# Optimization experiments

Measured on AMD Instinct MI355X. Metric: run time of the kernel, lower is better.

## Reference

```python
import jax, jax.numpy as jnp
import numpy as np

NUM_ITER = 5
NUM_SLOTS = 16
INPUT_SIZE = 256
EPS = 1e-8
TAU = 1.0
B, N = 8, 16384


def setup_inputs() -> dict:
    key = jax.random.key(0)
    k1, k2 = jax.random.split(key)
    inputs = jax.random.normal(k1, (B, N, INPUT_SIZE), dtype=jnp.float32)
    # xavier_uniform for a (1, K, D) tensor (torch fan_in=K*D, fan_out=D)
    limit = float(np.sqrt(6.0 / (NUM_SLOTS * INPUT_SIZE + INPUT_SIZE)))
    slot_logits = jax.random.uniform(k2, (1, NUM_SLOTS, INPUT_SIZE),
                                     minval=-limit, maxval=limit, dtype=jnp.float32)
    mixing_coefficients = jnp.full((1, NUM_SLOTS), 1.0 / NUM_SLOTS, dtype=jnp.float32)
    return {"inputs": inputs, "slot_logits": slot_logits,
            "mixing_coefficients": mixing_coefficients}


def reference(inputs, slot_logits, mixing_coefficients):
    Bn, Nn, D = inputs.shape
    theta = jnp.broadcast_to(slot_logits, (Bn, NUM_SLOTS, D))       # (B,K,D)
    pi = jnp.broadcast_to(mixing_coefficients, (Bn, NUM_SLOTS))     # (B,K)
    p = jax.nn.softmax(inputs, axis=-1)                             # (B,N,D), loop-invariant
    for _ in range(NUM_ITER):
        log_q = jax.nn.log_softmax(theta, axis=-1)                  # (B,K,D)
        logits = jnp.einsum('bnd,bkd->bnk', p, log_q)               # (B,N,K)
        logits = logits + jnp.log(pi + EPS)[:, None, :]
        gamma = jax.nn.softmax(logits, axis=-1)                     # (B,N,K)
        pi = gamma.mean(axis=1)                                     # (B,K)
        gamma_sum = gamma.sum(axis=1) + EPS                         # (B,K)
        numerator = jnp.einsum('bnk,bnd->bkd', gamma, inputs)       # (B,K,D)
        theta = numerator / gamma_sum[:, :, None]
    g = jax.random.gumbel(jax.random.key(1), theta.shape, dtype=theta.dtype)
    slots = jax.nn.softmax((theta + g) / TAU, axis=-1)              # (B,K,D)
    return slots
```

## Files before the change

### kernel.cpp

```cpp
#include <hip/hip_runtime.h>
#include <cstdint>
#include <cstddef>

#define BN 8
#define NN 16384
#define DD 256
#define KK 16
#define NITER 5
#define EPSV 1e-8f
#define LOG256 5.545177444479562f
#define PSTR 260
#define TPB 8
#define GG 64

typedef float f32x4 __attribute__((ext_vector_type(4)));
typedef long  i64v;

__device__ __forceinline__ float frcp(float x){ return __builtin_amdgcn_rcpf(x); }
__device__ __forceinline__ float wmax(float v){
  #pragma unroll
  for (int m = 32; m >= 1; m >>= 1) v = fmaxf(v, __shfl_xor(v, m, 64));
  return v;
}
__device__ __forceinline__ float wsum(float v){
  #pragma unroll
  for (int m = 32; m >= 1; m >>= 1) v += __shfl_xor(v, m, 64);
  return v;
}
__device__ __forceinline__ uint32_t pk4_fp8(float a, float b, float c, float d){
  int w = __builtin_amdgcn_cvt_pk_fp8_f32(a, b, 0, false);
  w = __builtin_amdgcn_cvt_pk_fp8_f32(c, d, w, true);
  return (uint32_t)w;
}
__device__ __forceinline__ uint32_t f2bf(float f){
  uint32_t u = __float_as_uint(f);
  return (u + 0x7fffu + ((u >> 16) & 1u)) >> 16;
}
__device__ __forceinline__ uint32_t pk2bf(float a, float b){
  return f2bf(a) | (f2bf(b) << 16);
}
__device__ __forceinline__ float bf2f(uint32_t h){ return __uint_as_float(h << 16); }

__global__ __launch_bounds__(256, 2) void k_prep6(const float* __restrict__ x,
                                                  uint2* __restrict__ pbf8,
                                                  uint2* __restrict__ xbf8,
                                                  float* __restrict__ invs){
  __shared__ float xs[2][32 * PSTR];
  const int b = blockIdx.y;
  const int Sbase = blockIdx.x * TPB;
  const int tid = threadIdx.x;
  const int wave = tid >> 6, lane = tid & 63;
  const float* xb = x + (size_t)b * NN * DD;

  auto stage = [&](int S, int buf){
    #pragma unroll
    for (int r = 0; r < 8; ++r){
      int row = wave * 8 + r;
      const float* gp = xb + ((size_t)S * 32 + row) * DD + lane * 4;
      float* lp = &xs[buf][row * PSTR];
      __builtin_amdgcn_global_load_lds(
          (const __attribute__((address_space(1))) unsigned int*)gp,
          (__attribute__((address_space(3))) unsigned int*)lp, 16, 0, 0);
    }
  };

  stage(Sbase, 0);
  for (int it = 0; it < TPB; ++it){
    const int S = Sbase + it;
    const int cur = it & 1;
    asm volatile("s_waitcnt vmcnt(0)" ::: "memory");
    __builtin_amdgcn_sched_barrier(0);
    __syncthreads();
    if (it + 1 < TPB) stage(S + 1, cur ^ 1);

    {
      int row = 8 * wave + (lane & 7);
      const float* pr = &xs[cur][row * PSTR + (lane >> 3) * 32];
      float a = 0.f;
      #pragma unroll
      for (int i = 0; i < 8; ++i){
        float4 v = *(const float4*)&pr[4 * i];
        a += __expf(v.x) + __expf(v.y) + __expf(v.z) + __expf(v.w);
      }
      a += __shfl_xor(a, 8, 64);
      a += __shfl_xor(a, 16, 64);
      a += __shfl_xor(a, 32, 64);
      if (lane < 8) invs[(size_t)b * NN + S * 32 + 8 * wave + lane] = frcp(a);
    }

    #pragma unroll
    for (int i = 0; i < 4; ++i){
      int p = wave * 4 + i; int c = p >> 3, s = p & 7;
      int rho = lane & 15;
      int n = 8 * (rho >> 2) + 4 * c + (rho & 3);
      int d = 32 * s + 8 * (lane >> 4);
      float4 v0 = *(const float4*)&xs[cur][n * PSTR + d];
      float4 v1 = *(const float4*)&xs[cur][n * PSTR + d + 4];
      uint2 o;
      o.x = pk4_fp8(__expf(v0.x), __expf(v0.y), __expf(v0.z), __expf(v0.w));
      o.y = pk4_fp8(__expf(v1.x), __expf(v1.y), __expf(v1.z), __expf(v1.w));
      pbf8[(((size_t)b * 1024 + (size_t)S * 2 + c) * 8 + s) * 64 + lane] = o;
    }
    #pragma unroll
    for (int i = 0; i < 4; ++i){
      int dt = wave * 4 + i;
      int col = dt * 16 + (lane & 15);
      int g2 = lane >> 4;
      float v[8];
      #pragma unroll
      for (int j = 0; j < 8; ++j) v[j] = xs[cur][(8 * g2 + j) * PSTR + col];
      uint2 o;
      o.x = pk4_fp8(v[0], v[1], v[2], v[3]);
      o.y = pk4_fp8(v[4], v[5], v[6], v[7]);
      xbf8[(((size_t)b * 512 + S) * 16 + dt) * 64 + lane] = o;
    }
    __syncthreads();
  }
}

__global__ __launch_bounds__(256) void k_init6(const float* __restrict__ slot_logits,
                                               const float* __restrict__ mix,
                                               uint8_t* __restrict__ lqf8,
                                               float* __restrict__ logpi){
  int w    = blockIdx.x * 4 + (threadIdx.x >> 6);
  int lane = threadIdx.x & 63;
  int b = w >> 4, k = w & 15;
  const float4* sl = (const float4*)(slot_logits + (size_t)k * DD);
  float4 t = sl[lane];
  float m = wmax(fmaxf(fmaxf(t.x, t.y), fmaxf(t.z, t.w)));
  float s = wsum(__expf(t.x-m) + __expf(t.y-m) + __expf(t.z-m) + __expf(t.w-m));
  float L = m + __logf(s) - LOG256;
  int d0 = lane * 4;
  int ss = d0 >> 5;
  int l2 = (((d0 & 31) >> 3) << 4) + k;
  int jb = d0 & 7;
  uint32_t wv = pk4_fp8(t.x - L, t.y - L, t.z - L, t.w - L);
  *(uint32_t*)(lqf8 + ((((size_t)b * 8 + ss) * 64 + l2) * 8 + jb)) = wv;
  if (lane == 0) logpi[w] = __logf(mix[k] + EPSV);
}

__global__ __launch_bounds__(256, 2) void k_em6(const uint2* __restrict__ pbf8,
                                                const uint2* __restrict__ xbf8,
                                                const uint2* __restrict__ lqf8,
                                                const float* __restrict__ logpi,
                                                const float* __restrict__ invs,
                                                uint16_t* __restrict__ pnumb,
                                                float* __restrict__ ppi){
  __shared__ float sred[KK * DD];
  __shared__ float spi2[16];
  const int b = blockIdx.y, g = blockIdx.x;
  const int tid = threadIdx.x;
  const int wave = tid >> 6, lane = tid & 63;

  i64v lq8[8];
  {
    const uint2* p = lqf8 + (size_t)b * 8 * 64 + lane;
    #pragma unroll
    for (int s = 0; s < 8; ++s){ uint2 t = p[s * 64]; lq8[s] = *(i64v*)&t; }
  }
  const float lpik = logpi[b * KK + (lane & 15)];

  f32x4 acc[16];
  #pragma unroll
  for (int dt = 0; dt < 16; ++dt) acc[dt] = (f32x4){0.f, 0.f, 0.f, 0.f};
  float piacc = 0.f;

  const int S0 = (g * 4 + wave) * 2;
  #pragma unroll
  for (int ssi = 0; ssi < 2; ++ssi){
    const int S = S0 + ssi;
    const uint2* pb = pbf8 + (((size_t)b * 1024 + (size_t)S * 2) * 8) * 64 + lane;
    const uint2* xr = xbf8 + (((size_t)b * 512 + S) * 16) * 64 + lane;

    uint2 pa[16];
    #pragma unroll
    for (int i = 0; i < 16; ++i) pa[i] = pb[(size_t)i * 64];

    float ivs[8];
    {
      const float* ib = invs + (size_t)b * NN + S * 32 + 8 * (lane >> 4);
      #pragma unroll
      for (int j = 0; j < 8; ++j) ivs[j] = ib[j];
    }

    float ga[8];
    #pragma unroll
    for (int c = 0; c < 2; ++c){
      f32x4 lc = (f32x4){0.f, 0.f, 0.f, 0.f};
      #pragma unroll
      for (int s = 0; s < 8; ++s){
        i64v a = *(i64v*)&pa[c * 8 + s];
        lc = __builtin_amdgcn_mfma_f32_16x16x32_fp8_fp8(a, lq8[s], lc, 0, 0, 0);
      }
      #pragma unroll
      for (int r2 = 0; r2 < 4; ++r2){
        float lg = fmaf(lc[r2], ivs[c * 4 + r2], lpik);
        float mx = lg;
        #pragma unroll
        for (int m = 1; m <= 8; m <<= 1) mx = fmaxf(mx, __shfl_xor(mx, m, 64));
        float e = __expf(lg - mx);
        float s2 = e;
        #pragma unroll
        for (int m = 1; m <= 8; m <<= 1) s2 += __shfl_xor(s2, m, 64);
        ga[c * 4 + r2] = e * frcp(s2);
      }
    }
    uint2 gp;
    gp.x = pk4_fp8(ga[0], ga[1], ga[2], ga[3]);
    gp.y = pk4_fp8(ga[4], ga[5], ga[6], ga[7]);
    piacc += __builtin_amdgcn_cvt_f32_fp8((int)gp.x, 0)
           + __builtin_amdgcn_cvt_f32_fp8((int)gp.x, 1)
           + __builtin_amdgcn_cvt_f32_fp8((int)gp.x, 2)
           + __builtin_amdgcn_cvt_f32_fp8((int)gp.x, 3)
           + __builtin_amdgcn_cvt_f32_fp8((int)gp.y, 0)
           + __builtin_amdgcn_cvt_f32_fp8((int)gp.y, 1)
           + __builtin_amdgcn_cvt_f32_fp8((int)gp.y, 2)
           + __builtin_amdgcn_cvt_f32_fp8((int)gp.y, 3);
    i64v gA = *(i64v*)&gp;
    #pragma unroll
    for (int dt = 0; dt < 16; ++dt){
      uint2 xv = xr[(size_t)dt * 64];
      acc[dt] = __builtin_amdgcn_mfma_f32_16x16x32_fp8_fp8(gA, *(i64v*)&xv,
                                                           acc[dt], 0, 0, 0);
    }
  }

  float pk = piacc;
  pk += __shfl_xor(pk, 16, 64);
  pk += __shfl_xor(pk, 32, 64);
  __syncthreads();
  if (wave == 0){
    #pragma unroll
    for (int dt = 0; dt < 16; ++dt)
      #pragma unroll
      for (int r2 = 0; r2 < 4; ++r2)
        sred[(4 * (lane >> 4) + r2) * DD + dt * 16 + (lane & 15)] = acc[dt][r2];
    if (lane < 16) spi2[lane] = pk;
  }
  __syncthreads();
  for (int w = 1; w < 4; ++w){
    if (wave == w){
      #pragma unroll
      for (int dt = 0; dt < 16; ++dt)
        #pragma unroll
        for (int r2 = 0; r2 < 4; ++r2)
          sred[(4 * (lane >> 4) + r2) * DD + dt * 16 + (lane & 15)] += acc[dt][r2];
      if (lane < 16) spi2[lane] += pk;
    }
    __syncthreads();
  }
  uint32_t* dst = (uint32_t*)(pnumb + (size_t)(b * GG + g) * KK * DD);
  #pragma unroll
  for (int j = 0; j < 8; ++j){
    float a = sred[tid * 2 + j * 512];
    float c = sred[tid * 2 + 1 + j * 512];
    dst[tid + j * 256] = pk2bf(a, c);
  }
  if (tid < 16) ppi[(size_t)(b * GG + g) * KK + tid] = spi2[tid];
}

__global__ __launch_bounds__(64) void k_reduce6(const uint16_t* __restrict__ pnumb,
                                                const float* __restrict__ ppi,
                                                float* __restrict__ theta,
                                                uint8_t* __restrict__ lqf8,
                                                float* __restrict__ logpi){
  int w = blockIdx.x;
  int lane = threadIdx.x;
  int b = w >> 4, k = w & 15;
  float4 sum = make_float4(0.f, 0.f, 0.f, 0.f);
  #pragma unroll 4
  for (int g = 0; g < GG; ++g){
    const uint2* p = (const uint2*)(pnumb +
        ((size_t)(b * GG + g) * KK + k) * DD + lane * 4);
    uint2 v = *p;
    sum.x += bf2f(v.x & 0xffffu); sum.y += bf2f(v.x >> 16);
    sum.z += bf2f(v.y & 0xffffu); sum.w += bf2f(v.y >> 16);
  }
  float ps = 0.f;
  for (int g = lane; g < GG; g += 64) ps += ppi[((size_t)b * GG + g) * KK + k];
  ps = wsum(ps);
  float inv = frcp(ps + EPSV);
  float4 th = make_float4(sum.x * inv, sum.y * inv, sum.z * inv, sum.w * inv);
  ((float4*)(theta + (size_t)w * DD))[lane] = th;
  float m = wmax(fmaxf(fmaxf(th.x, th.y), fmaxf(th.z, th.w)));
  float s = wsum(__expf(th.x-m) + __expf(th.y-m) + __expf(th.z-m) + __expf(th.w-m));
  float L = m + __logf(s) - LOG256;
  int d0 = lane * 4;
  int ss = d0 >> 5;
  int l2 = (((d0 & 31) >> 3) << 4) + k;
  int jb = d0 & 7;
  uint32_t wv = pk4_fp8(th.x - L, th.y - L, th.z - L, th.w - L);
  *(uint32_t*)(lqf8 + ((((size_t)b * 8 + ss) * 64 + l2) * 8 + jb)) = wv;
  if (lane == 0) logpi[w] = __logf(ps * (1.0f / NN) + EPSV);
}

__device__ __forceinline__ uint32_t rotl32(uint32_t x, int r){ return (x << r) | (x >> (32 - r)); }
__device__ __forceinline__ void tf2x32(uint32_t k0, uint32_t k1, uint32_t c0, uint32_t c1,
                                       uint32_t& o0, uint32_t& o1){
  uint32_t ks0 = k0, ks1 = k1, ks2 = 0x1BD11BDAu ^ k0 ^ k1;
  uint32_t x0 = c0 + ks0, x1 = c1 + ks1;
  #define RND(r) { x0 += x1; x1 = rotl32(x1, r); x1 ^= x0; }
  RND(13) RND(15) RND(26) RND(6)   x0 += ks1; x1 += ks2 + 1u;
  RND(17) RND(29) RND(16) RND(24)  x0 += ks2; x1 += ks0 + 2u;
  RND(13) RND(15) RND(26) RND(6)   x0 += ks0; x1 += ks1 + 3u;
  RND(17) RND(29) RND(16) RND(24)  x0 += ks1; x1 += ks2 + 4u;
  RND(13) RND(15) RND(26) RND(6)   x0 += ks2; x1 += ks0 + 5u;
  #undef RND
  o0 = x0; o1 = x1;
}

__global__ __launch_bounds__(256) void k_final(const float* __restrict__ theta,
                                               float* __restrict__ out){
  int w    = blockIdx.x * 4 + (threadIdx.x >> 6);
  int lane = threadIdx.x & 63;
  float4 th = ((const float4*)(theta + (size_t)w * DD))[lane];
  int i0 = w * DD + lane * 4;
  float gv[4];
  #pragma unroll
  for (int j = 0; j < 4; ++j){
    uint32_t i = (uint32_t)(i0 + j);
    uint32_t o0, o1;
    tf2x32(0u, 1u, 0u, i, o0, o1);
    uint32_t bits = o0 ^ o1;
    float f = __uint_as_float((bits >> 9) | 0x3f800000u) - 1.0f;
    const float TINY = 1.17549435e-38f;
    float u = fmaxf(f + TINY, TINY);
    gv[j] = -logf(-logf(u));
  }
  float4 y = make_float4(th.x + gv[0], th.y + gv[1], th.z + gv[2], th.w + gv[3]);
  float m = wmax(fmaxf(fmaxf(y.x, y.y), fmaxf(y.z, y.w)));
  float4 e = make_float4(__expf(y.x-m), __expf(y.y-m), __expf(y.z-m), __expf(y.w-m));
  float s = wsum(e.x + e.y + e.z + e.w);
  float inv = 1.0f / s;
  ((float4*)(out + (size_t)w * DD))[lane] =
      make_float4(e.x*inv, e.y*inv, e.z*inv, e.w*inv);
}

__global__ __launch_bounds__(256) void k_fill(float* __restrict__ out, float v){
  out[blockIdx.x * 256 + threadIdx.x] = v;
}

extern "C" void kernel_launch(void* const* d_in, const int* in_sizes, int n_in,
                              void* d_out, int out_size, void* d_ws, size_t ws_size,
                              hipStream_t stream){
  const float* x    = (const float*)d_in[0];
  const float* sl   = (const float*)d_in[1];
  const float* mix  = (const float*)d_in[2];
  float* out = (float*)d_out;
  char* ws = (char*)d_ws;

  const size_t SZ_PBF  = 33554432ull;
  const size_t SZ_XBF  = 33554432ull;
  const size_t SZ_LQF  = 32768ull;
  const size_t SZ_INV  = (size_t)BN*NN*4;
  const size_t SZ_TH   = (size_t)BN*KK*DD*4;
  const size_t SZ_LP   = 512ull;
  const size_t SZ_PNUM = (size_t)BN*GG*KK*DD*2;
  const size_t SZ_PPI  = (size_t)BN*GG*KK*4;
  size_t need = SZ_PBF + SZ_XBF + SZ_LQF + SZ_INV + SZ_TH + SZ_LP + SZ_PNUM + SZ_PPI;

  if (ws_size < need){
    k_fill<<<(BN*KK*DD)/256, 256, 0, stream>>>(out, -9.0f);
    return;
  }
  size_t o = 0;
  uint2*    pbf8  = (uint2*)(ws + o);     o += SZ_PBF;
  uint2*    xbf8  = (uint2*)(ws + o);     o += SZ_XBF;
  uint8_t*  lqf8  = (uint8_t*)(ws + o);   o += SZ_LQF;
  float*    invs  = (float*)(ws + o);     o += SZ_INV;
  float*    theta = (float*)(ws + o);     o += SZ_TH;
  float*    logpi = (float*)(ws + o);     o += SZ_LP;
  uint16_t* pnumb = (uint16_t*)(ws + o);  o += SZ_PNUM;
  float*    ppi   = (float*)(ws + o);

  k_prep6<<<dim3(512 / TPB, BN), 256, 0, stream>>>(x, pbf8, xbf8, invs);
  k_init6<<<(BN*KK)/4, 256, 0, stream>>>(sl, mix, lqf8, logpi);
  for (int it = 0; it < NITER; ++it){
    k_em6    <<<dim3(GG, BN), 256, 0, stream>>>(pbf8, xbf8, (const uint2*)lqf8,
                                                logpi, invs, pnumb, ppi);
    k_reduce6<<<BN*KK, 64, 0, stream>>>(pnumb, ppi, theta, lqf8, logpi);
  }
  k_final<<<(BN*KK)/4, 256, 0, stream>>>(theta, out);
}
```

Baseline: 161.5 us.

## Fuse per-iteration reduction and final softmax into EM kernel via last-block counter

The separate reduce and final kernels are folded into the EM kernel. The last block to finish for each batch, detected with an atomic counter and thread fences, does the cross-block reduction, updates log_q and log_pi, and on the last iteration applies the Gumbel softmax directly. This removes six kernel launches and the theta buffer, at the cost of a serial tail where one block per batch does all 16 row reductions. Separately, the prep kernel drops its LDS double buffering and raises its occupancy hint from 2 to 4 blocks, relying on more resident blocks rather than in-block prefetch to hide load latency.

```diff
diff --git a/kernel.cpp b/kernel.cpp
--- a/kernel.cpp
+++ b/kernel.cpp
@@ -41,41 +41,35 @@
 }
 __device__ __forceinline__ float bf2f(uint32_t h){ return __uint_as_float(h << 16); }
 
-__global__ __launch_bounds__(256, 2) void k_prep6(const float* __restrict__ x,
+__global__ __launch_bounds__(256, 4) void k_prep6(const float* __restrict__ x,
                                                   uint2* __restrict__ pbf8,
                                                   uint2* __restrict__ xbf8,
                                                   float* __restrict__ invs){
-  __shared__ float xs[2][32 * PSTR];
+  __shared__ float xs[32 * PSTR];
   const int b = blockIdx.y;
   const int Sbase = blockIdx.x * TPB;
   const int tid = threadIdx.x;
   const int wave = tid >> 6, lane = tid & 63;
   const float* xb = x + (size_t)b * NN * DD;
 
-  auto stage = [&](int S, int buf){
+  for (int it = 0; it < TPB; ++it){
+    const int S = Sbase + it;
     #pragma unroll
     for (int r = 0; r < 8; ++r){
       int row = wave * 8 + r;
       const float* gp = xb + ((size_t)S * 32 + row) * DD + lane * 4;
-      float* lp = &xs[buf][row * PSTR];
+      float* lp = &xs[row * PSTR];
       __builtin_amdgcn_global_load_lds(
           (const __attribute__((address_space(1))) unsigned int*)gp,
           (__attribute__((address_space(3))) unsigned int*)lp, 16, 0, 0);
     }
-  };
-
-  stage(Sbase, 0);
-  for (int it = 0; it < TPB; ++it){
-    const int S = Sbase + it;
-    const int cur = it & 1;
     asm volatile("s_waitcnt vmcnt(0)" ::: "memory");
     __builtin_amdgcn_sched_barrier(0);
     __syncthreads();
-    if (it + 1 < TPB) stage(S + 1, cur ^ 1);
 
     {
       int row = 8 * wave + (lane & 7);
-      const float* pr = &xs[cur][row * PSTR + (lane >> 3) * 32];
+      const float* pr = &xs[row * PSTR + (lane >> 3) * 32];
       float a = 0.f;
       #pragma unroll
       for (int i = 0; i < 8; ++i){
@@ -87,15 +81,14 @@
       a += __shfl_xor(a, 32, 64);
       if (lane < 8) invs[(size_t)b * NN + S * 32 + 8 * wave + lane] = frcp(a);
     }
-
     #pragma unroll
     for (int i = 0; i < 4; ++i){
       int p = wave * 4 + i; int c = p >> 3, s = p & 7;
       int rho = lane & 15;
       int n = 8 * (rho >> 2) + 4 * c + (rho & 3);
       int d = 32 * s + 8 * (lane >> 4);
-      float4 v0 = *(const float4*)&xs[cur][n * PSTR + d];
-      float4 v1 = *(const float4*)&xs[cur][n * PSTR + d + 4];
+      float4 v0 = *(const float4*)&xs[n * PSTR + d];
+      float4 v1 = *(const float4*)&xs[n * PSTR + d + 4];
       uint2 o;
       o.x = pk4_fp8(__expf(v0.x), __expf(v0.y), __expf(v0.z), __expf(v0.w));
       o.y = pk4_fp8(__expf(v1.x), __expf(v1.y), __expf(v1.z), __expf(v1.w));
@@ -108,7 +101,7 @@
       int g2 = lane >> 4;
       float v[8];
       #pragma unroll
-      for (int j = 0; j < 8; ++j) v[j] = xs[cur][(8 * g2 + j) * PSTR + col];
+      for (int j = 0; j < 8; ++j) v[j] = xs[(8 * g2 + j) * PSTR + col];
       uint2 o;
       o.x = pk4_fp8(v[0], v[1], v[2], v[3]);
       o.y = pk4_fp8(v[4], v[5], v[6], v[7]);
@@ -139,161 +132,6 @@
   if (lane == 0) logpi[w] = __logf(mix[k] + EPSV);
 }
 
-__global__ __launch_bounds__(256, 2) void k_em6(const uint2* __restrict__ pbf8,
-                                                const uint2* __restrict__ xbf8,
-                                                const uint2* __restrict__ lqf8,
-                                                const float* __restrict__ logpi,
-                                                const float* __restrict__ invs,
-                                                uint16_t* __restrict__ pnumb,
-                                                float* __restrict__ ppi){
-  __shared__ float sred[KK * DD];
-  __shared__ float spi2[16];
-  const int b = blockIdx.y, g = blockIdx.x;
-  const int tid = threadIdx.x;
-  const int wave = tid >> 6, lane = tid & 63;
-
-  i64v lq8[8];
-  {
-    const uint2* p = lqf8 + (size_t)b * 8 * 64 + lane;
-    #pragma unroll
-    for (int s = 0; s < 8; ++s){ uint2 t = p[s * 64]; lq8[s] = *(i64v*)&t; }
-  }
-  const float lpik = logpi[b * KK + (lane & 15)];
-
-  f32x4 acc[16];
-  #pragma unroll
-  for (int dt = 0; dt < 16; ++dt) acc[dt] = (f32x4){0.f, 0.f, 0.f, 0.f};
-  float piacc = 0.f;
-
-  const int S0 = (g * 4 + wave) * 2;
-  #pragma unroll
-  for (int ssi = 0; ssi < 2; ++ssi){
-    const int S = S0 + ssi;
-    const uint2* pb = pbf8 + (((size_t)b * 1024 + (size_t)S * 2) * 8) * 64 + lane;
-    const uint2* xr = xbf8 + (((size_t)b * 512 + S) * 16) * 64 + lane;
-
-    uint2 pa[16];
-    #pragma unroll
-    for (int i = 0; i < 16; ++i) pa[i] = pb[(size_t)i * 64];
-
-    float ivs[8];
-    {
-      const float* ib = invs + (size_t)b * NN + S * 32 + 8 * (lane >> 4);
-      #pragma unroll
-      for (int j = 0; j < 8; ++j) ivs[j] = ib[j];
-    }
-
-    float ga[8];
-    #pragma unroll
-    for (int c = 0; c < 2; ++c){
-      f32x4 lc = (f32x4){0.f, 0.f, 0.f, 0.f};
-      #pragma unroll
-      for (int s = 0; s < 8; ++s){
-        i64v a = *(i64v*)&pa[c * 8 + s];
-        lc = __builtin_amdgcn_mfma_f32_16x16x32_fp8_fp8(a, lq8[s], lc, 0, 0, 0);
-      }
-      #pragma unroll
-      for (int r2 = 0; r2 < 4; ++r2){
-        float lg = fmaf(lc[r2], ivs[c * 4 + r2], lpik);
-        float mx = lg;
-        #pragma unroll
-        for (int m = 1; m <= 8; m <<= 1) mx = fmaxf(mx, __shfl_xor(mx, m, 64));
-        float e = __expf(lg - mx);
-        float s2 = e;
-        #pragma unroll
-        for (int m = 1; m <= 8; m <<= 1) s2 += __shfl_xor(s2, m, 64);
-        ga[c * 4 + r2] = e * frcp(s2);
-      }
-    }
-    uint2 gp;
-    gp.x = pk4_fp8(ga[0], ga[1], ga[2], ga[3]);
-    gp.y = pk4_fp8(ga[4], ga[5], ga[6], ga[7]);
-    piacc += __builtin_amdgcn_cvt_f32_fp8((int)gp.x, 0)
-           + __builtin_amdgcn_cvt_f32_fp8((int)gp.x, 1)
-           + __builtin_amdgcn_cvt_f32_fp8((int)gp.x, 2)
-           + __builtin_amdgcn_cvt_f32_fp8((int)gp.x, 3)
-           + __builtin_amdgcn_cvt_f32_fp8((int)gp.y, 0)
-           + __builtin_amdgcn_cvt_f32_fp8((int)gp.y, 1)
-           + __builtin_amdgcn_cvt_f32_fp8((int)gp.y, 2)
-           + __builtin_amdgcn_cvt_f32_fp8((int)gp.y, 3);
-    i64v gA = *(i64v*)&gp;
-    #pragma unroll
-    for (int dt = 0; dt < 16; ++dt){
-      uint2 xv = xr[(size_t)dt * 64];
-      acc[dt] = __builtin_amdgcn_mfma_f32_16x16x32_fp8_fp8(gA, *(i64v*)&xv,
-                                                           acc[dt], 0, 0, 0);
-    }
-  }
-
-  float pk = piacc;
-  pk += __shfl_xor(pk, 16, 64);
-  pk += __shfl_xor(pk, 32, 64);
-  __syncthreads();
-  if (wave == 0){
-    #pragma unroll
-    for (int dt = 0; dt < 16; ++dt)
-      #pragma unroll
-      for (int r2 = 0; r2 < 4; ++r2)
-        sred[(4 * (lane >> 4) + r2) * DD + dt * 16 + (lane & 15)] = acc[dt][r2];
-    if (lane < 16) spi2[lane] = pk;
-  }
-  __syncthreads();
-  for (int w = 1; w < 4; ++w){
-    if (wave == w){
-      #pragma unroll
-      for (int dt = 0; dt < 16; ++dt)
-        #pragma unroll
-        for (int r2 = 0; r2 < 4; ++r2)
-          sred[(4 * (lane >> 4) + r2) * DD + dt * 16 + (lane & 15)] += acc[dt][r2];
-      if (lane < 16) spi2[lane] += pk;
-    }
-    __syncthreads();
-  }
-  uint32_t* dst = (uint32_t*)(pnumb + (size_t)(b * GG + g) * KK * DD);
-  #pragma unroll
-  for (int j = 0; j < 8; ++j){
-    float a = sred[tid * 2 + j * 512];
-    float c = sred[tid * 2 + 1 + j * 512];
-    dst[tid + j * 256] = pk2bf(a, c);
-  }
-  if (tid < 16) ppi[(size_t)(b * GG + g) * KK + tid] = spi2[tid];
-}
-
-__global__ __launch_bounds__(64) void k_reduce6(const uint16_t* __restrict__ pnumb,
-                                                const float* __restrict__ ppi,
-                                                float* __restrict__ theta,
-                                                uint8_t* __restrict__ lqf8,
-                                                float* __restrict__ logpi){
-  int w = blockIdx.x;
-  int lane = threadIdx.x;
-  int b = w >> 4, k = w & 15;
-  float4 sum = make_float4(0.f, 0.f, 0.f, 0.f);
-  #pragma unroll 4
-  for (int g = 0; g < GG; ++g){
-    const uint2* p = (const uint2*)(pnumb +
-        ((size_t)(b * GG + g) * KK + k) * DD + lane * 4);
-    uint2 v = *p;
-    sum.x += bf2f(v.x & 0xffffu); sum.y += bf2f(v.x >> 16);
-    sum.z += bf2f(v.y & 0xffffu); sum.w += bf2f(v.y >> 16);
-  }
-  float ps = 0.f;
-  for (int g = lane; g < GG; g += 64) ps += ppi[((size_t)b * GG + g) * KK + k];
-  ps = wsum(ps);
-  float inv = frcp(ps + EPSV);
-  float4 th = make_float4(sum.x * inv, sum.y * inv, sum.z * inv, sum.w * inv);
-  ((float4*)(theta + (size_t)w * DD))[lane] = th;
-  float m = wmax(fmaxf(fmaxf(th.x, th.y), fmaxf(th.z, th.w)));
-  float s = wsum(__expf(th.x-m) + __expf(th.y-m) + __expf(th.z-m) + __expf(th.w-m));
-  float L = m + __logf(s) - LOG256;
-  int d0 = lane * 4;
-  int ss = d0 >> 5;
-  int l2 = (((d0 & 31) >> 3) << 4) + k;
-  int jb = d0 & 7;
-  uint32_t wv = pk4_fp8(th.x - L, th.y - L, th.z - L, th.w - L);
-  *(uint32_t*)(lqf8 + ((((size_t)b * 8 + ss) * 64 + l2) * 8 + jb)) = wv;
-  if (lane == 0) logpi[w] = __logf(ps * (1.0f / NN) + EPSV);
-}
-
 __device__ __forceinline__ uint32_t rotl32(uint32_t x, int r){ return (x << r) | (x >> (32 - r)); }
 __device__ __forceinline__ void tf2x32(uint32_t k0, uint32_t k1, uint32_t c0, uint32_t c1,
                                        uint32_t& o0, uint32_t& o1){
@@ -309,11 +147,39 @@
   o0 = x0; o1 = x1;
 }
 
-__global__ __launch_bounds__(256) void k_final(const float* __restrict__ theta,
-                                               float* __restrict__ out){
-  int w    = blockIdx.x * 4 + (threadIdx.x >> 6);
-  int lane = threadIdx.x & 63;
-  float4 th = ((const float4*)(theta + (size_t)w * DD))[lane];
+__device__ __forceinline__ void dev_reduce_row(const uint16_t* __restrict__ pnumb,
+    const float* __restrict__ ppi, uint8_t* __restrict__ lqf8,
+    float* __restrict__ logpi, float* __restrict__ out,
+    int b, int k, int lane, int dofinal){
+  int w = b * KK + k;
+  float4 sum = make_float4(0.f, 0.f, 0.f, 0.f);
+  #pragma unroll 4
+  for (int g = 0; g < GG; ++g){
+    const uint2* p = (const uint2*)(pnumb +
+        ((size_t)(b * GG + g) * KK + k) * DD + lane * 4);
+    uint2 v = *p;
+    sum.x += bf2f(v.x & 0xffffu); sum.y += bf2f(v.x >> 16);
+    sum.z += bf2f(v.y & 0xffffu); sum.w += bf2f(v.y >> 16);
+  }
+  float ps = 0.f;
+  for (int g = lane; g < GG; g += 64) ps += ppi[((size_t)b * GG + g) * KK + k];
+  ps = wsum(ps);
+  float inv = frcp(ps + EPSV);
+  float4 th = make_float4(sum.x * inv, sum.y * inv, sum.z * inv, sum.w * inv);
+
+  if (!dofinal){
+    float m = wmax(fmaxf(fmaxf(th.x, th.y), fmaxf(th.z, th.w)));
+    float s = wsum(__expf(th.x-m) + __expf(th.y-m) + __expf(th.z-m) + __expf(th.w-m));
+    float L = m + __logf(s) - LOG256;
+    int d0 = lane * 4;
+    int ss = d0 >> 5;
+    int l2 = (((d0 & 31) >> 3) << 4) + k;
+    int jb = d0 & 7;
+    uint32_t wv = pk4_fp8(th.x - L, th.y - L, th.z - L, th.w - L);
+    *(uint32_t*)(lqf8 + ((((size_t)b * 8 + ss) * 64 + l2) * 8 + jb)) = wv;
+    if (lane == 0) logpi[w] = __logf(ps * (1.0f / NN) + EPSV);
+    return;
+  }
   int i0 = w * DD + lane * 4;
   float gv[4];
   #pragma unroll
@@ -331,9 +197,144 @@
   float m = wmax(fmaxf(fmaxf(y.x, y.y), fmaxf(y.z, y.w)));
   float4 e = make_float4(__expf(y.x-m), __expf(y.y-m), __expf(y.z-m), __expf(y.w-m));
   float s = wsum(e.x + e.y + e.z + e.w);
-  float inv = 1.0f / s;
+  float invq = 1.0f / s;
   ((float4*)(out + (size_t)w * DD))[lane] =
-      make_float4(e.x*inv, e.y*inv, e.z*inv, e.w*inv);
+      make_float4(e.x*invq, e.y*invq, e.z*invq, e.w*invq);
+}
+
+__global__ __launch_bounds__(256, 2) void k_em7(const uint2* __restrict__ pbf8,
+                                                const uint2* __restrict__ xbf8,
+                                                const uint2* __restrict__ lqf8v,
+                                                const float* __restrict__ logpi,
+                                                const float* __restrict__ invs,
+                                                uint16_t* __restrict__ pnumb,
+                                                float* __restrict__ ppi,
+                                                uint8_t* __restrict__ lqf8,
+                                                float* __restrict__ logpi_w,
+                                                float* __restrict__ out,
+                                                uint32_t* __restrict__ cnt,
+                                                int dofinal){
+  __shared__ float sred[KK * DD];
+  __shared__ float spi2[16];
+  __shared__ int amlast;
+  const int b = blockIdx.y, g = blockIdx.x;
+  const int tid = threadIdx.x;
+  const int wave = tid >> 6, lane = tid & 63;
+
+  i64v lq8[8];
+  {
+    const uint2* p = lqf8v + (size_t)b * 8 * 64 + lane;
+    #pragma unroll
+    for (int s = 0; s < 8; ++s){ uint2 t = p[s * 64]; lq8[s] = *(i64v*)&t; }
+  }
+  const float lpik = logpi[b * KK + (lane & 15)];
+
+  f32x4 acc[16];
+  #pragma unroll
+  for (int dt = 0; dt < 16; ++dt) acc[dt] = (f32x4){0.f, 0.f, 0.f, 0.f};
+  float piacc = 0.f;
+
+  const int S0 = (g * 4 + wave) * 2;
+  #pragma unroll
+  for (int ssi = 0; ssi < 2; ++ssi){
+    const int S = S0 + ssi;
+    const uint2* pb = pbf8 + (((size_t)b * 1024 + (size_t)S * 2) * 8) * 64 + lane;
+    const uint2* xr = xbf8 + (((size_t)b * 512 + S) * 16) * 64 + lane;
+    uint2 pa[16];
+    #pragma unroll
+    for (int i = 0; i < 16; ++i) pa[i] = pb[(size_t)i * 64];
+    float ivs[8];
+    {
+      const float* ib = invs + (size_t)b * NN + S * 32 + 8 * (lane >> 4);
+      #pragma unroll
+      for (int j = 0; j < 8; ++j) ivs[j] = ib[j];
+    }
+    float ga[8];
+    #pragma unroll
+    for (int c = 0; c < 2; ++c){
+      f32x4 lc = (f32x4){0.f, 0.f, 0.f, 0.f};
+      #pragma unroll
+      for (int s = 0; s < 8; ++s){
+        i64v a = *(i64v*)&pa[c * 8 + s];
+        lc = __builtin_amdgcn_mfma_f32_16x16x32_fp8_fp8(a, lq8[s], lc, 0, 0, 0);
+      }
+      #pragma unroll
+      for (int r2 = 0; r2 < 4; ++r2){
+        float lg = fmaf(lc[r2], ivs[c * 4 + r2], lpik);
+        float mx = lg;
+        #pragma unroll
+        for (int m = 1; m <= 8; m <<= 1) mx = fmaxf(mx, __shfl_xor(mx, m, 64));
+        float e = __expf(lg - mx);
+        float s2 = e;
+        #pragma unroll
+        for (int m = 1; m <= 8; m <<= 1) s2 += __shfl_xor(s2, m, 64);
+        ga[c * 4 + r2] = e * frcp(s2);
+      }
+    }
+    uint2 gp;
+    gp.x = pk4_fp8(ga[0], ga[1], ga[2], ga[3]);
+    gp.y = pk4_fp8(ga[4], ga[5], ga[6], ga[7]);
+    piacc += __builtin_amdgcn_cvt_f32_fp8((int)gp.x, 0)
+           + __builtin_amdgcn_cvt_f32_fp8((int)gp.x, 1)
+           + __builtin_amdgcn_cvt_f32_fp8((int)gp.x, 2)
+           + __builtin_amdgcn_cvt_f32_fp8((int)gp.x, 3)
+           + __builtin_amdgcn_cvt_f32_fp8((int)gp.y, 0)
+           + __builtin_amdgcn_cvt_f32_fp8((int)gp.y, 1)
+           + __builtin_amdgcn_cvt_f32_fp8((int)gp.y, 2)
+           + __builtin_amdgcn_cvt_f32_fp8((int)gp.y, 3);
+    i64v gA = *(i64v*)&gp;
+    #pragma unroll
+    for (int dt = 0; dt < 16; ++dt){
+      uint2 xv = xr[(size_t)dt * 64];
+      acc[dt] = __builtin_amdgcn_mfma_f32_16x16x32_fp8_fp8(gA, *(i64v*)&xv,
+                                                           acc[dt], 0, 0, 0);
+    }
+  }
+
+  float pk = piacc;
+  pk += __shfl_xor(pk, 16, 64);
+  pk += __shfl_xor(pk, 32, 64);
+  __syncthreads();
+  if (wave == 0){
+    #pragma unroll
+    for (int dt = 0; dt < 16; ++dt)
+      #pragma unroll
+      for (int r2 = 0; r2 < 4; ++r2)
+        sred[(4 * (lane >> 4) + r2) * DD + dt * 16 + (lane & 15)] = acc[dt][r2];
+    if (lane < 16) spi2[lane] = pk;
+  }
+  __syncthreads();
+  for (int w = 1; w < 4; ++w){
+    if (wave == w){
+      #pragma unroll
+      for (int dt = 0; dt < 16; ++dt)
+        #pragma unroll
+        for (int r2 = 0; r2 < 4; ++r2)
+          sred[(4 * (lane >> 4) + r2) * DD + dt * 16 + (lane & 15)] += acc[dt][r2];
+      if (lane < 16) spi2[lane] += pk;
+    }
+    __syncthreads();
+  }
+  uint32_t* dst = (uint32_t*)(pnumb + (size_t)(b * GG + g) * KK * DD);
+  #pragma unroll
+  for (int j = 0; j < 8; ++j){
+    float a = sred[tid * 2 + j * 512];
+    float c = sred[tid * 2 + 1 + j * 512];
+    dst[tid + j * 256] = pk2bf(a, c);
+  }
+  if (tid < 16) ppi[(size_t)(b * GG + g) * KK + tid] = spi2[tid];
+
+  __threadfence();
+  if (tid == 0){
+    uint32_t old = atomicAdd(&cnt[b], 1u);
+    amlast = (old == (uint32_t)(GG - 1)) ? 1 : 0;
+  }
+  __syncthreads();
+  if (!amlast) return;
+  __threadfence();
+  #pragma unroll
+  for (int j = 0; j < 4; ++j)
+    dev_reduce_row(pnumb, ppi, lqf8, logpi_w, out, b, wave * 4 + j, lane, dofinal);
 }
 
 __global__ __launch_bounds__(256) void k_fill(float* __restrict__ out, float v){
@@ -353,11 +354,11 @@
   const size_t SZ_XBF  = 33554432ull;
   const size_t SZ_LQF  = 32768ull;
   const size_t SZ_INV  = (size_t)BN*NN*4;
-  const size_t SZ_TH   = (size_t)BN*KK*DD*4;
   const size_t SZ_LP   = 512ull;
   const size_t SZ_PNUM = (size_t)BN*GG*KK*DD*2;
   const size_t SZ_PPI  = (size_t)BN*GG*KK*4;
-  size_t need = SZ_PBF + SZ_XBF + SZ_LQF + SZ_INV + SZ_TH + SZ_LP + SZ_PNUM + SZ_PPI;
+  const size_t SZ_CNT  = (size_t)NITER*BN*4;
+  size_t need = SZ_PBF + SZ_XBF + SZ_LQF + SZ_INV + SZ_LP + SZ_PNUM + SZ_PPI + SZ_CNT;
 
   if (ws_size < need){
     k_fill<<<(BN*KK*DD)/256, 256, 0, stream>>>(out, -9.0f);
@@ -368,17 +369,19 @@
   uint2*    xbf8  = (uint2*)(ws + o);     o += SZ_XBF;
   uint8_t*  lqf8  = (uint8_t*)(ws + o);   o += SZ_LQF;
   float*    invs  = (float*)(ws + o);     o += SZ_INV;
-  float*    theta = (float*)(ws + o);     o += SZ_TH;
   float*    logpi = (float*)(ws + o);     o += SZ_LP;
   uint16_t* pnumb = (uint16_t*)(ws + o);  o += SZ_PNUM;
-  float*    ppi   = (float*)(ws + o);
-
+  float*    ppi   = (float*)(ws + o);     o += SZ_PPI;
+  uint32_t* cnt   = (uint32_t*)(ws + o);
+
+  hipMemsetAsync(cnt, 0, SZ_CNT, stream);
   k_prep6<<<dim3(512 / TPB, BN), 256, 0, stream>>>(x, pbf8, xbf8, invs);
   k_init6<<<(BN*KK)/4, 256, 0, stream>>>(sl, mix, lqf8, logpi);
   for (int it = 0; it < NITER; ++it){
-    k_em6    <<<dim3(GG, BN), 256, 0, stream>>>(pbf8, xbf8, (const uint2*)lqf8,
-                                                logpi, invs, pnumb, ppi);
-    k_reduce6<<<BN*KK, 64, 0, stream>>>(pnumb, ppi, theta, lqf8, logpi);
-  }
-  k_final<<<(BN*KK)/4, 256, 0, stream>>>(theta, out);
-}
+    k_em7<<<dim3(GG, BN), 256, 0, stream>>>(pbf8, xbf8, (const uint2*)lqf8,
+                                            logpi, invs, pnumb, ppi,
+                                            lqf8, logpi, out,
+                                            cnt + (size_t)it * BN,
+                                            (it == NITER - 1) ? 1 : 0);
+  }
+}
```

Result: slower. 498.4 us (+208.7%).

## Fuse final gumbel-softmax into last reduce; single-buffer prep LDS for occupancy

Applied to the files above, without the earlier changes.

The final Gumbel-softmax kernel is folded into the last k_reduce6 launch through a dofinal flag. This removes one kernel launch and the theta round trip through global memory. Separately, k_prep6 drops its LDS double-buffering and raises launch bounds from 2 to 4 blocks per CU, relying on more resident blocks to hide load latency in place of explicit prefetch. The risk is that prep loses its intra-block overlap of loads and compute.

```diff
diff --git a/kernel.cpp b/kernel.cpp
--- a/kernel.cpp
+++ b/kernel.cpp
@@ -41,41 +41,35 @@
 }
 __device__ __forceinline__ float bf2f(uint32_t h){ return __uint_as_float(h << 16); }
 
-__global__ __launch_bounds__(256, 2) void k_prep6(const float* __restrict__ x,
+__global__ __launch_bounds__(256, 4) void k_prep6(const float* __restrict__ x,
                                                   uint2* __restrict__ pbf8,
                                                   uint2* __restrict__ xbf8,
                                                   float* __restrict__ invs){
-  __shared__ float xs[2][32 * PSTR];
+  __shared__ float xs[32 * PSTR];
   const int b = blockIdx.y;
   const int Sbase = blockIdx.x * TPB;
   const int tid = threadIdx.x;
   const int wave = tid >> 6, lane = tid & 63;
   const float* xb = x + (size_t)b * NN * DD;
 
-  auto stage = [&](int S, int buf){
+  for (int it = 0; it < TPB; ++it){
+    const int S = Sbase + it;
     #pragma unroll
     for (int r = 0; r < 8; ++r){
       int row = wave * 8 + r;
       const float* gp = xb + ((size_t)S * 32 + row) * DD + lane * 4;
-      float* lp = &xs[buf][row * PSTR];
+      float* lp = &xs[row * PSTR];
       __builtin_amdgcn_global_load_lds(
           (const __attribute__((address_space(1))) unsigned int*)gp,
           (__attribute__((address_space(3))) unsigned int*)lp, 16, 0, 0);
     }
-  };
-
-  stage(Sbase, 0);
-  for (int it = 0; it < TPB; ++it){
-    const int S = Sbase + it;
-    const int cur = it & 1;
     asm volatile("s_waitcnt vmcnt(0)" ::: "memory");
     __builtin_amdgcn_sched_barrier(0);
     __syncthreads();
-    if (it + 1 < TPB) stage(S + 1, cur ^ 1);
 
     {
       int row = 8 * wave + (lane & 7);
-      const float* pr = &xs[cur][row * PSTR + (lane >> 3) * 32];
+      const float* pr = &xs[row * PSTR + (lane >> 3) * 32];
       float a = 0.f;
       #pragma unroll
       for (int i = 0; i < 8; ++i){
@@ -87,15 +81,14 @@
       a += __shfl_xor(a, 32, 64);
       if (lane < 8) invs[(size_t)b * NN + S * 32 + 8 * wave + lane] = frcp(a);
     }
-
     #pragma unroll
     for (int i = 0; i < 4; ++i){
       int p = wave * 4 + i; int c = p >> 3, s = p & 7;
       int rho = lane & 15;
       int n = 8 * (rho >> 2) + 4 * c + (rho & 3);
       int d = 32 * s + 8 * (lane >> 4);
-      float4 v0 = *(const float4*)&xs[cur][n * PSTR + d];
-      float4 v1 = *(const float4*)&xs[cur][n * PSTR + d + 4];
+      float4 v0 = *(const float4*)&xs[n * PSTR + d];
+      float4 v1 = *(const float4*)&xs[n * PSTR + d + 4];
       uint2 o;
       o.x = pk4_fp8(__expf(v0.x), __expf(v0.y), __expf(v0.z), __expf(v0.w));
       o.y = pk4_fp8(__expf(v1.x), __expf(v1.y), __expf(v1.z), __expf(v1.w));
@@ -108,7 +101,7 @@
       int g2 = lane >> 4;
       float v[8];
       #pragma unroll
-      for (int j = 0; j < 8; ++j) v[j] = xs[cur][(8 * g2 + j) * PSTR + col];
+      for (int j = 0; j < 8; ++j) v[j] = xs[(8 * g2 + j) * PSTR + col];
       uint2 o;
       o.x = pk4_fp8(v[0], v[1], v[2], v[3]);
       o.y = pk4_fp8(v[4], v[5], v[6], v[7]);
@@ -259,41 +252,6 @@
   if (tid < 16) ppi[(size_t)(b * GG + g) * KK + tid] = spi2[tid];
 }
 
-__global__ __launch_bounds__(64) void k_reduce6(const uint16_t* __restrict__ pnumb,
-                                                const float* __restrict__ ppi,
-                                                float* __restrict__ theta,
-                                                uint8_t* __restrict__ lqf8,
-                                                float* __restrict__ logpi){
-  int w = blockIdx.x;
-  int lane = threadIdx.x;
-  int b = w >> 4, k = w & 15;
-  float4 sum = make_float4(0.f, 0.f, 0.f, 0.f);
-  #pragma unroll 4
-  for (int g = 0; g < GG; ++g){
-    const uint2* p = (const uint2*)(pnumb +
-        ((size_t)(b * GG + g) * KK + k) * DD + lane * 4);
-    uint2 v = *p;
-    sum.x += bf2f(v.x & 0xffffu); sum.y += bf2f(v.x >> 16);
-    sum.z += bf2f(v.y & 0xffffu); sum.w += bf2f(v.y >> 16);
-  }
-  float ps = 0.f;
-  for (int g = lane; g < GG; g += 64) ps += ppi[((size_t)b * GG + g) * KK + k];
-  ps = wsum(ps);
-  float inv = frcp(ps + EPSV);
-  float4 th = make_float4(sum.x * inv, sum.y * inv, sum.z * inv, sum.w * inv);
-  ((float4*)(theta + (size_t)w * DD))[lane] = th;
-  float m = wmax(fmaxf(fmaxf(th.x, th.y), fmaxf(th.z, th.w)));
-  float s = wsum(__expf(th.x-m) + __expf(th.y-m) + __expf(th.z-m) + __expf(th.w-m));
-  float L = m + __logf(s) - LOG256;
-  int d0 = lane * 4;
-  int ss = d0 >> 5;
-  int l2 = (((d0 & 31) >> 3) << 4) + k;
-  int jb = d0 & 7;
-  uint32_t wv = pk4_fp8(th.x - L, th.y - L, th.z - L, th.w - L);
-  *(uint32_t*)(lqf8 + ((((size_t)b * 8 + ss) * 64 + l2) * 8 + jb)) = wv;
-  if (lane == 0) logpi[w] = __logf(ps * (1.0f / NN) + EPSV);
-}
-
 __device__ __forceinline__ uint32_t rotl32(uint32_t x, int r){ return (x << r) | (x >> (32 - r)); }
 __device__ __forceinline__ void tf2x32(uint32_t k0, uint32_t k1, uint32_t c0, uint32_t c1,
                                        uint32_t& o0, uint32_t& o1){
@@ -309,11 +267,41 @@
   o0 = x0; o1 = x1;
 }
 
-__global__ __launch_bounds__(256) void k_final(const float* __restrict__ theta,
-                                               float* __restrict__ out){
-  int w    = blockIdx.x * 4 + (threadIdx.x >> 6);
-  int lane = threadIdx.x & 63;
-  float4 th = ((const float4*)(theta + (size_t)w * DD))[lane];
+__global__ __launch_bounds__(64) void k_reduce6(const uint16_t* __restrict__ pnumb,
+    const float* __restrict__ ppi, uint8_t* __restrict__ lqf8,
+    float* __restrict__ logpi, float* __restrict__ out, int dofinal){
+  int w = blockIdx.x;
+  int lane = threadIdx.x;
+  int b = w >> 4, k = w & 15;
+  float4 sum = make_float4(0.f, 0.f, 0.f, 0.f);
+  #pragma unroll 4
+  for (int g = 0; g < GG; ++g){
+    const uint2* p = (const uint2*)(pnumb +
+        ((size_t)(b * GG + g) * KK + k) * DD + lane * 4);
+    uint2 v = *p;
+    sum.x += bf2f(v.x & 0xffffu); sum.y += bf2f(v.x >> 16);
+    sum.z += bf2f(v.y & 0xffffu); sum.w += bf2f(v.y >> 16);
+  }
+  float ps = 0.f;
+  for (int g = lane; g < GG; g += 64) ps += ppi[((size_t)b * GG + g) * KK + k];
+  ps = wsum(ps);
+  float inv = frcp(ps + EPSV);
+  float4 th = make_float4(sum.x * inv, sum.y * inv, sum.z * inv, sum.w * inv);
+
+  if (!dofinal){
+    float m = wmax(fmaxf(fmaxf(th.x, th.y), fmaxf(th.z, th.w)));
+    float s = wsum(__expf(th.x-m) + __expf(th.y-m) + __expf(th.z-m) + __expf(th.w-m));
+    float L = m + __logf(s) - LOG256;
+    int d0 = lane * 4;
+    int ss = d0 >> 5;
+    int l2 = (((d0 & 31) >> 3) << 4) + k;
+    int jb = d0 & 7;
+    uint32_t wv = pk4_fp8(th.x - L, th.y - L, th.z - L, th.w - L);
+    *(uint32_t*)(lqf8 + ((((size_t)b * 8 + ss) * 64 + l2) * 8 + jb)) = wv;
+    if (lane == 0) logpi[w] = __logf(ps * (1.0f / NN) + EPSV);
+    return;
+  }
+
   int i0 = w * DD + lane * 4;
   float gv[4];
   #pragma unroll
@@ -331,9 +319,9 @@
   float m = wmax(fmaxf(fmaxf(y.x, y.y), fmaxf(y.z, y.w)));
   float4 e = make_float4(__expf(y.x-m), __expf(y.y-m), __expf(y.z-m), __expf(y.w-m));
   float s = wsum(e.x + e.y + e.z + e.w);
-  float inv = 1.0f / s;
+  float invq = 1.0f / s;
   ((float4*)(out + (size_t)w * DD))[lane] =
-      make_float4(e.x*inv, e.y*inv, e.z*inv, e.w*inv);
+      make_float4(e.x*invq, e.y*invq, e.z*invq, e.w*invq);
 }
 
 __global__ __launch_bounds__(256) void k_fill(float* __restrict__ out, float v){
@@ -353,11 +341,10 @@
   const size_t SZ_XBF  = 33554432ull;
   const size_t SZ_LQF  = 32768ull;
   const size_t SZ_INV  = (size_t)BN*NN*4;
-  const size_t SZ_TH   = (size_t)BN*KK*DD*4;
   const size_t SZ_LP   = 512ull;
   const size_t SZ_PNUM = (size_t)BN*GG*KK*DD*2;
   const size_t SZ_PPI  = (size_t)BN*GG*KK*4;
-  size_t need = SZ_PBF + SZ_XBF + SZ_LQF + SZ_INV + SZ_TH + SZ_LP + SZ_PNUM + SZ_PPI;
+  size_t need = SZ_PBF + SZ_XBF + SZ_LQF + SZ_INV + SZ_LP + SZ_PNUM + SZ_PPI;
 
   if (ws_size < need){
     k_fill<<<(BN*KK*DD)/256, 256, 0, stream>>>(out, -9.0f);
@@ -368,7 +355,6 @@
   uint2*    xbf8  = (uint2*)(ws + o);     o += SZ_XBF;
   uint8_t*  lqf8  = (uint8_t*)(ws + o);   o += SZ_LQF;
   float*    invs  = (float*)(ws + o);     o += SZ_INV;
-  float*    theta = (float*)(ws + o);     o += SZ_TH;
   float*    logpi = (float*)(ws + o);     o += SZ_LP;
   uint16_t* pnumb = (uint16_t*)(ws + o);  o += SZ_PNUM;
   float*    ppi   = (float*)(ws + o);
@@ -376,9 +362,9 @@
   k_prep6<<<dim3(512 / TPB, BN), 256, 0, stream>>>(x, pbf8, xbf8, invs);
   k_init6<<<(BN*KK)/4, 256, 0, stream>>>(sl, mix, lqf8, logpi);
   for (int it = 0; it < NITER; ++it){
-    k_em6    <<<dim3(GG, BN), 256, 0, stream>>>(pbf8, xbf8, (const uint2*)lqf8,
-                                                logpi, invs, pnumb, ppi);
-    k_reduce6<<<BN*KK, 64, 0, stream>>>(pnumb, ppi, theta, lqf8, logpi);
-  }
-  k_final<<<(BN*KK)/4, 256, 0, stream>>>(theta, out);
-}
+    k_em6<<<dim3(GG, BN), 256, 0, stream>>>(pbf8, xbf8, (const uint2*)lqf8,
+                                            logpi, invs, pnumb, ppi);
+    k_reduce6<<<BN*KK, 64, 0, stream>>>(pnumb, ppi, lqf8, logpi, out,
+                                        (it == NITER - 1) ? 1 : 0);
+  }
+}
```

Result: no change. 159.2 us (-1.4%).
